# Kernel optimization log

Hardware: AMD Instinct MI355X
Metric: run time of the kernel (lower is better)

The kernel has to match this reference:

```python
import jax, jax.numpy as jnp
import numpy as np
from jax import lax

RATIO = 0.25
K = 32


def setup_inputs() -> dict:
    key = jax.random.key(0)
    ks = jax.random.split(key, 5)
    B, N, C = 16, 4096, 64
    pos = jax.random.normal(ks[0], (B, N, 3), jnp.float32)
    x = jax.random.normal(ks[1], (B, N, C), jnp.float32)

    def lin(k, fan_in, fan_out):
        return jax.random.normal(k, (fan_in, fan_out), jnp.float32) / np.sqrt(fan_in).astype(np.float32)

    W1 = lin(ks[2], C + 3, 128); b1 = jnp.zeros((128,), jnp.float32)
    W2 = lin(ks[3], 128, 128);   b2 = jnp.zeros((128,), jnp.float32)
    W3 = lin(ks[4], 128, 256);   b3 = jnp.zeros((256,), jnp.float32)
    return dict(x=x, pos=pos, W1=W1, b1=b1, W2=W2, b2=b2, W3=W3, b3=b3)


def _fps(pos, M):
    """Iterative farthest point sampling on one cloud. pos: [N,3] -> idx [M]."""
    N = pos.shape[0]

    def step(carry, _):
        dists, last = carry
        d = jnp.sum((pos - pos[last]) ** 2, axis=-1)      # [N]
        dists = jnp.minimum(dists, d)
        nxt = jnp.argmax(dists).astype(jnp.int32)
        return (dists, nxt), last

    init = (jnp.full((N,), 1e30, pos.dtype), jnp.int32(0))
    _, idx = lax.scan(step, init, None, length=M)
    return idx  # first emitted index is 0, then farthest points in order


def reference(x, pos, W1, b1, W2, b2, W3, b3):
    B, N, _ = pos.shape
    M = int(N * RATIO)

    # --- FPS sampling per cloud ---
    idx = jax.vmap(lambda p: _fps(p, M))(pos)                        # [B,M] int32
    pos_s = jnp.take_along_axis(pos, idx[..., None], axis=1)          # [B,M,3]

    # --- kNN graph: K nearest source points for each sampled centroid ---
    d2 = jnp.sum((pos_s[:, :, None, :] - pos[:, None, :, :]) ** 2, -1)  # [B,M,N]
    _, nidx = lax.top_k(-d2, K)                                       # [B,M,K]

    # --- gather neighbor features & relative positions ---
    x_j = jax.vmap(lambda xb, ib: xb[ib])(x, nidx)                    # [B,M,K,C]
    pos_j = jax.vmap(lambda pb, ib: pb[ib])(pos, nidx)                # [B,M,K,3]
    rel = pos_j - pos_s[:, :, None, :]                                # [B,M,K,3]

    # --- PointNetConv: local MLP on [x_j || rel], max aggregation ---
    msg = jnp.concatenate([x_j, rel], axis=-1)                        # [B,M,K,C+3]
    h = jax.nn.relu(msg @ W1 + b1)
    h = jax.nn.relu(h @ W2 + b2)
    h = jax.nn.relu(h @ W3 + b3)                                      # [B,M,K,256]
    out = jnp.max(h, axis=2)                                          # [B,M,256]
    return out, pos_s
```

## Files before the change

kernel.cpp:

```cpp
#include <hip/hip_runtime.h>


#define B_    16
#define N_    4096
#define M_    1024
#define AST   136
#define NWORK 240
#define NITEM (256 * 16)

typedef __bf16 bf16x8 __attribute__((ext_vector_type(8)));
typedef __bf16 bf16x4 __attribute__((ext_vector_type(4)));
typedef float  f32x4  __attribute__((ext_vector_type(4)));
typedef float  f32x2  __attribute__((ext_vector_type(2)));

__global__ __launch_bounds__(256) void prep_weights(
    const float* __restrict__ W1, const float* __restrict__ W2,
    const float* __restrict__ W3,
    __bf16* __restrict__ w1t, __bf16* __restrict__ w2t, __bf16* __restrict__ w3t) {
  const int t = blockIdx.x * 256 + threadIdx.x;
  if (t < 128 * 96) {
    const int n = t / 96, k = t % 96;
    w1t[t] = (k < 67) ? (__bf16)W1[k * 128 + n] : (__bf16)0.0f;
  }
  if (t < 128 * 128) {
    const int n = t >> 7, k = t & 127;
    w2t[t] = (__bf16)W2[k * 128 + n];
  }
  {
    const int n = t >> 7, k = t & 127;
    w3t[t] = (__bf16)W3[k * 256 + n];
  }
}

__device__ __forceinline__ f32x2 pk_sub(f32x2 a, f32x2 b) {
  f32x2 d;
  asm("v_pk_add_f32 %0, %1, %2 neg_lo:[0,1] neg_hi:[0,1]" : "=v"(d) : "v"(a), "v"(b));
  return d;
}
__device__ __forceinline__ f32x2 pk_mul(f32x2 a, f32x2 b) {
  f32x2 d;
  asm("v_pk_mul_f32 %0, %1, %2" : "=v"(d) : "v"(a), "v"(b));
  return d;
}
__device__ __forceinline__ f32x2 pk_add(f32x2 a, f32x2 b) {
  f32x2 d;
  asm("v_pk_add_f32 %0, %1, %2" : "=v"(d) : "v"(a), "v"(b));
  return d;
}

__device__ __forceinline__ double mk_key(float d, unsigned lo) {
  unsigned long long k = ((unsigned long long)__float_as_uint(d) << 32) | lo;
  return __builtin_bit_cast(double, k);
}

template <int CTRL>
__device__ __forceinline__ double dpp_max_f64(double v) {
  unsigned long long k = __builtin_bit_cast(unsigned long long, v);
  unsigned lo = (unsigned)__builtin_amdgcn_update_dpp(0, (int)(unsigned)k,         CTRL, 0xF, 0xF, true);
  unsigned hi = (unsigned)__builtin_amdgcn_update_dpp(0, (int)(unsigned)(k >> 32), CTRL, 0xF, 0xF, true);
  double p = __builtin_bit_cast(double, ((unsigned long long)hi << 32) | lo);
  return fmax(v, p);
}

union ShU {
  struct { float4 pp[N_]; unsigned long long sw[2][4]; } f;
  struct { __bf16 A[128 * AST]; __bf16 Bv[128 * AST]; } g;
};

__global__ __launch_bounds__(256) void fused_kernel(
    const float* __restrict__ pos, const float* __restrict__ x,
    const float* __restrict__ b1, const float* __restrict__ b2,
    const float* __restrict__ b3,
    const __bf16* __restrict__ w1t, const __bf16* __restrict__ w2t,
    const __bf16* __restrict__ w3t,
    int* __restrict__ ipub, int* __restrict__ ctr,
    float* __restrict__ out, float* __restrict__ pos_s) {
  __shared__ alignas(16) ShU sh;
  __shared__ int sh_item;
  const int tid = threadIdx.x;

  if (blockIdx.x < B_) {
    __builtin_amdgcn_s_setprio(3);
    const int b = blockIdx.x;
    const float* pb = pos + (size_t)b * N_ * 3;
    for (int i = tid; i < N_; i += 256)
      sh.f.pp[i] = make_float4(pb[3 * i], pb[3 * i + 1], pb[3 * i + 2], 0.0f);
    __syncthreads();

    f32x2 X2[8], Y2[8], Z2[8];
    float D[16];
    unsigned lo16[16];
    const unsigned ntid = ~(unsigned)tid;
#pragma unroll
    for (int j = 0; j < 8; j++) {
      float4 p0 = sh.f.pp[tid + ((2 * j) << 8)];
      float4 p1 = sh.f.pp[tid + ((2 * j + 1) << 8)];
      X2[j][0] = p0.x; X2[j][1] = p1.x;
      Y2[j][0] = p0.y; Y2[j][1] = p1.y;
      Z2[j][0] = p0.z; Z2[j][1] = p1.z;
      D[2 * j] = 1e30f; D[2 * j + 1] = 1e30f;
      lo16[2 * j]     = ntid - (unsigned)((2 * j) << 8);
      lo16[2 * j + 1] = ntid - (unsigned)((2 * j + 1) << 8);
    }

    float4 q = sh.f.pp[0];
    if (tid == 0) {
      __hip_atomic_store(ipub + b * M_, 1, __ATOMIC_RELAXED,
                         __HIP_MEMORY_SCOPE_AGENT);
      float* o = pos_s + (size_t)b * M_ * 3;
      o[0] = q.x; o[1] = q.y; o[2] = q.z;
    }

    for (int i = 1; i < M_; i++) {
      f32x2 qx; qx[0] = q.x; qx[1] = q.x;
      f32x2 qy; qy[0] = q.y; qy[1] = q.y;
      f32x2 qz; qz[0] = q.z; qz[1] = q.z;
      double key[16];
#pragma unroll
      for (int j = 0; j < 8; j++) {
        f32x2 dx = pk_sub(X2[j], qx);
        f32x2 dy = pk_sub(Y2[j], qy);
        f32x2 dz = pk_sub(Z2[j], qz);
        f32x2 t0 = pk_mul(dx, dx);
        f32x2 t1 = pk_mul(dy, dy);
        f32x2 s  = pk_add(t0, t1);
        f32x2 t2 = pk_mul(dz, dz);
        f32x2 d2 = pk_add(s, t2);
        D[2 * j]     = fminf(D[2 * j],     d2[0]);
        D[2 * j + 1] = fminf(D[2 * j + 1], d2[1]);
        key[2 * j]     = mk_key(D[2 * j],     lo16[2 * j]);
        key[2 * j + 1] = mk_key(D[2 * j + 1], lo16[2 * j + 1]);
      }
#pragma unroll
      for (int s = 8; s > 0; s >>= 1)
#pragma unroll
        for (int k = 0; k < s; k++)
          key[k] = fmax(key[k], key[k + s]);
      double kk = key[0];

      kk = dpp_max_f64<0xB1>(kk);
      kk = dpp_max_f64<0x4E>(kk);
      kk = dpp_max_f64<0x141>(kk);
      kk = dpp_max_f64<0x140>(kk);
      kk = dpp_max_f64<0x142>(kk);
      kk = dpp_max_f64<0x143>(kk);

      const int par = i & 1;
      if ((tid & 63) == 63)
        sh.f.sw[par][tid >> 6] = __builtin_bit_cast(unsigned long long, kk);
      asm volatile("s_waitcnt lgkmcnt(0)" ::: "memory");
      __builtin_amdgcn_s_barrier();

      const ulonglong2 v01 = *(const ulonglong2*)&sh.f.sw[par][0];
      const ulonglong2 v23 = *(const ulonglong2*)&sh.f.sw[par][2];
      const int c0 = (int)(~(unsigned)v01.x), c1 = (int)(~(unsigned)v01.y);
      const int c2 = (int)(~(unsigned)v23.x), c3 = (int)(~(unsigned)v23.y);
      float4 q0 = sh.f.pp[c0], q1 = sh.f.pp[c1], q2 = sh.f.pp[c2], q3 = sh.f.pp[c3];
      unsigned long long k01, k23; float4 q01, q23; int i01, i23;
      if (v01.y > v01.x) { k01 = v01.y; q01 = q1; i01 = c1; }
      else               { k01 = v01.x; q01 = q0; i01 = c0; }
      if (v23.y > v23.x) { k23 = v23.y; q23 = q3; i23 = c3; }
      else               { k23 = v23.x; q23 = q2; i23 = c2; }
      int cur;
      if (k23 > k01) { q = q23; cur = i23; }
      else           { q = q01; cur = i01; }

      if (tid == 0) {
        __hip_atomic_store(ipub + b * M_ + i, cur + 1, __ATOMIC_RELAXED,
                           __HIP_MEMORY_SCOPE_AGENT);
        float* o = pos_s + ((size_t)b * M_ + i) * 3;
        o[0] = q.x; o[1] = q.y; o[2] = q.z;
      }
    }
    return;
  }

  const int w    = tid >> 6;
  const int lane = tid & 63;

  for (;;) {
    if (tid == 0) sh_item = atomicAdd(ctr, 1);
    __syncthreads();
    const int it = sh_item;
    if (it >= NITEM) return;
    const int b    = it & 15;
    const int mset = it >> 4;
    const int m    = mset * 4 + w;

    __syncthreads();
    {
      const float* pb = pos + (size_t)b * N_ * 3;
      for (int i = tid; i < N_; i += 256)
        sh.f.pp[i] = make_float4(pb[3 * i], pb[3 * i + 1], pb[3 * i + 2], 0.0f);
    }
    __syncthreads();

    int ci0 = 0;
    if (lane == 0) {
      int v;
      while ((v = __hip_atomic_load(ipub + b * M_ + m, __ATOMIC_RELAXED,
                                    __HIP_MEMORY_SCOPE_AGENT)) == 0)
        __builtin_amdgcn_s_sleep(8);
      ci0 = v - 1;
    }
    const int ci = __shfl(ci0, 0);
    const float4 c = sh.f.pp[ci];

    float d2v[64];
    unsigned long long kmin = ~0ull;
#pragma unroll
    for (int t = 0; t < 64; t++) {
      const int j = t * 64 + lane;
      const float4 p = sh.f.pp[j];
      float dx = __fsub_rn(p.x, c.x);
      float dy = __fsub_rn(p.y, c.y);
      float dz = __fsub_rn(p.z, c.z);
      float d  = __fadd_rn(__fadd_rn(__fmul_rn(dx, dx), __fmul_rn(dy, dy)),
                           __fmul_rn(dz, dz));
      d2v[t] = d;
      const unsigned long long k64 =
          ((unsigned long long)__float_as_uint(d) << 32) | (unsigned int)j;
      if (k64 < kmin) kmin = k64;
    }

    unsigned long long sk = kmin;
#pragma unroll
    for (int size = 2; size <= 64; size <<= 1) {
#pragma unroll
      for (int stride = size >> 1; stride > 0; stride >>= 1) {
        const unsigned long long other = __shfl_xor(sk, stride);
        const bool up      = ((lane & size) == 0);
        const bool lowhalf = ((lane & stride) == 0);
        const bool takeMin = (up == lowhalf);
        const bool swp     = takeMin ? (other < sk) : (other > sk);
        if (swp) sk = other;
      }
    }
    const unsigned long long T0 = __shfl(sk, 31);
    const bool seeded = (kmin <= T0);

    unsigned long long rkey = (lane < 32) ? sk : ~0ull;
    unsigned long long wk   = T0;

#pragma unroll
    for (int t = 0; t < 64; t++) {
      const int j = t * 64 + lane;
      const unsigned long long k64 =
          ((unsigned long long)__float_as_uint(d2v[t]) << 32) | (unsigned int)j;
      const bool skip = seeded && (k64 == kmin);
      unsigned long long mask = __ballot((k64 < wk) && !skip);
      if (mask) {
        while (mask) {
          const int src = __ffsll((unsigned long long)mask) - 1;
          mask &= mask - 1;
          const unsigned long long cand = __shfl(k64, src);
          const int pos_i = (int)__popcll(__ballot(rkey < cand));
          const unsigned long long sh_ = __shfl_up(rkey, 1);
          if (lane < 32) {
            if (lane == pos_i)      rkey = cand;
            else if (lane > pos_i)  rkey = sh_;
          }
        }
        wk = __shfl(rkey, 31);
      }
    }
    const int njl = (int)(rkey & 0xFFFFull);
    __syncthreads();

    {
      const int rl   = lane >> 1;
      const int half = lane & 1;
      const int r    = w * 32 + rl;
      const int nj   = __shfl(njl, rl);
      const float4* xr = (const float4*)(x + ((size_t)(b * N_ + nj)) * 64 + half * 32);
      __bf16* dst = &sh.g.A[r * AST + half * 32];
#pragma unroll
      for (int t = 0; t < 8; t++) {
        float4 v = xr[t];
        bf16x4 u;
        u[0] = (__bf16)v.x; u[1] = (__bf16)v.y; u[2] = (__bf16)v.z; u[3] = (__bf16)v.w;
        *(bf16x4*)(dst + t * 4) = u;
      }
      bf16x8 z;
#pragma unroll
      for (int q2 = 0; q2 < 8; q2++) z[q2] = (__bf16)0.0f;
      if (half == 0) {
        const float* pj = pos + ((size_t)(b * N_ + nj)) * 3;
        bf16x8 u = z;
        u[0] = (__bf16)(pj[0] - c.x);
        u[1] = (__bf16)(pj[1] - c.y);
        u[2] = (__bf16)(pj[2] - c.z);
        *(bf16x8*)&sh.g.A[r * AST + 64] = u;
        *(bf16x8*)&sh.g.A[r * AST + 72] = z;
      } else {
        *(bf16x8*)&sh.g.A[r * AST + 80] = z;
        *(bf16x8*)&sh.g.A[r * AST + 88] = z;
      }
    }
    __syncthreads();

    const int lrow = lane & 15;
    const int lk8  = (lane >> 4) << 3;
    const int orow = (lane >> 4) << 2;

    {
      f32x4 acc[8][2];
#pragma unroll
      for (int n = 0; n < 2; n++) {
        const float bv = b1[(2 * w + n) * 16 + lrow];
        f32x4 a = {bv, bv, bv, bv};
#pragma unroll
        for (int rt = 0; rt < 8; rt++) acc[rt][n] = a;
      }
#pragma unroll
      for (int s = 0; s < 3; s++) {
        bf16x8 a[8];
#pragma unroll
        for (int rt = 0; rt < 8; rt++)
          a[rt] = *(const bf16x8*)&sh.g.A[(rt * 16 + lrow) * AST + s * 32 + lk8];
#pragma unroll
        for (int n = 0; n < 2; n++) {
          bf16x8 bb = *(const bf16x8*)&w1t[((2 * w + n) * 16 + lrow) * 96 + s * 32 + lk8];
#pragma unroll
          for (int rt = 0; rt < 8; rt++)
            acc[rt][n] = __builtin_amdgcn_mfma_f32_16x16x32_bf16(a[rt], bb, acc[rt][n], 0, 0, 0);
        }
      }
      __syncthreads();
#pragma unroll
      for (int n = 0; n < 2; n++)
#pragma unroll
        for (int rt = 0; rt < 8; rt++)
#pragma unroll
          for (int j = 0; j < 4; j++)
            sh.g.Bv[(rt * 16 + orow + j) * AST + (2 * w + n) * 16 + lrow] =
                (__bf16)fmaxf(acc[rt][n][j], 0.0f);
    }
    __syncthreads();

    {
      f32x4 acc[8][2];
#pragma unroll
      for (int n = 0; n < 2; n++) {
        const float bv = b2[(2 * w + n) * 16 + lrow];
        f32x4 a = {bv, bv, bv, bv};
#pragma unroll
        for (int rt = 0; rt < 8; rt++) acc[rt][n] = a;
      }
#pragma unroll
      for (int s = 0; s < 4; s++) {
        bf16x8 a[8];
#pragma unroll
        for (int rt = 0; rt < 8; rt++)
          a[rt] = *(const bf16x8*)&sh.g.Bv[(rt * 16 + lrow) * AST + s * 32 + lk8];
#pragma unroll
        for (int n = 0; n < 2; n++) {
          bf16x8 bb = *(const bf16x8*)&w2t[((2 * w + n) * 16 + lrow) * 128 + s * 32 + lk8];
#pragma unroll
          for (int rt = 0; rt < 8; rt++)
            acc[rt][n] = __builtin_amdgcn_mfma_f32_16x16x32_bf16(a[rt], bb, acc[rt][n], 0, 0, 0);
        }
      }
      __syncthreads();
#pragma unroll
      for (int n = 0; n < 2; n++)
#pragma unroll
        for (int rt = 0; rt < 8; rt++)
#pragma unroll
          for (int j = 0; j < 4; j++)
            sh.g.A[(rt * 16 + orow + j) * AST + (2 * w + n) * 16 + lrow] =
                (__bf16)fmaxf(acc[rt][n][j], 0.0f);
    }
    __syncthreads();

#pragma unroll
    for (int np = 0; np < 2; np++) {
      f32x4 acc[8][2];
#pragma unroll
      for (int n = 0; n < 2; n++) {
        const float bv = b3[(4 * w + 2 * np + n) * 16 + lrow];
        f32x4 a = {bv, bv, bv, bv};
#pragma unroll
        for (int rt = 0; rt < 8; rt++) acc[rt][n] = a;
      }
#pragma unroll
      for (int s = 0; s < 4; s++) {
        bf16x8 a[8];
#pragma unroll
        for (int rt = 0; rt < 8; rt++)
          a[rt] = *(const bf16x8*)&sh.g.A[(rt * 16 + lrow) * AST + s * 32 + lk8];
#pragma unroll
        for (int n = 0; n < 2; n++) {
          bf16x8 bb = *(const bf16x8*)&w3t[((4 * w + 2 * np + n) * 16 + lrow) * 128 + s * 32 + lk8];
#pragma unroll
          for (int rt = 0; rt < 8; rt++)
            acc[rt][n] = __builtin_amdgcn_mfma_f32_16x16x32_bf16(a[rt], bb, acc[rt][n], 0, 0, 0);
        }
      }
#pragma unroll
      for (int ccc = 0; ccc < 4; ccc++) {
#pragma unroll
        for (int n = 0; n < 2; n++) {
          f32x4 a0 = acc[2 * ccc][n], a1 = acc[2 * ccc + 1][n];
          float v = fmaxf(fmaxf(fmaxf(a0[0], a0[1]), fmaxf(a0[2], a0[3])),
                          fmaxf(fmaxf(a1[0], a1[1]), fmaxf(a1[2], a1[3])));
          v = fmaxf(v, __shfl_xor(v, 16));
          v = fmaxf(v, __shfl_xor(v, 32));
          v = fmaxf(v, 0.0f);
          if (lane < 16)
            out[((size_t)(b * M_ + mset * 4 + ccc)) * 256 + (4 * w + 2 * np + n) * 16 + lane] = v;
        }
      }
    }
  }
}

extern "C" void kernel_launch(void* const* d_in, const int* in_sizes, int n_in,
                              void* d_out, int out_size, void* d_ws, size_t ws_size,
                              hipStream_t stream) {
  const float* x   = (const float*)d_in[0];
  const float* pos = (const float*)d_in[1];
  const float* W1  = (const float*)d_in[2];
  const float* b1  = (const float*)d_in[3];
  const float* W2  = (const float*)d_in[4];
  const float* b2  = (const float*)d_in[5];
  const float* W3  = (const float*)d_in[6];
  const float* b3  = (const float*)d_in[7];

  float* out   = (float*)d_out;
  float* pos_s = out + (size_t)B_ * M_ * 256;

  char* ws = (char*)d_ws;
  int*    ipub = (int*)ws;
  int*    ctr  = (int*)(ws + 65536);
  __bf16* w1t  = (__bf16*)(ws + 65792);
  __bf16* w2t  = (__bf16*)(ws + 90368);
  __bf16* w3t  = (__bf16*)(ws + 123136);

  hipMemsetAsync(ws, 0, 65540, stream);
  prep_weights<<<dim3(128), dim3(256), 0, stream>>>(W1, W2, W3, w1t, w2t, w3t);
  fused_kernel<<<dim3(B_ + NWORK), dim3(256), 0, stream>>>(
      pos, x, b1, b2, b3, w1t, w2t, w3t, ipub, ctr, out, pos_s);
}
```

Baseline: 597.8 us.

## Process final centroid group in FPS block and simplify winner selection

Measured after the change: 594.2 us. About the same (-0.6%).

```diff
diff --git a/kernel.cpp b/kernel.cpp
--- a/kernel.cpp
+++ b/kernel.cpp
@@ -6,7 +6,7 @@
 #define M_    1024
 #define AST   136
 #define NWORK 240
-#define NITEM (256 * 16)
+#define NITEM (255 * 16)
 
 typedef __bf16 bf16x8 __attribute__((ext_vector_type(8)));
 typedef __bf16 bf16x4 __attribute__((ext_vector_type(4)));
@@ -66,6 +66,225 @@
   struct { float4 pp[N_]; unsigned long long sw[2][4]; } f;
   struct { __bf16 A[128 * AST]; __bf16 Bv[128 * AST]; } g;
 };
+
+__device__ __forceinline__ void process_item(
+    ShU& sh, int tid, int b, int mset, int ci,
+    const float* __restrict__ x, const float* __restrict__ pos,
+    const float* __restrict__ b1, const float* __restrict__ b2,
+    const float* __restrict__ b3,
+    const __bf16* __restrict__ w1t, const __bf16* __restrict__ w2t,
+    const __bf16* __restrict__ w3t, float* __restrict__ out) {
+  const int w    = tid >> 6;
+  const int lane = tid & 63;
+  const float4 c = sh.f.pp[ci];
+
+  float d2v[64];
+  unsigned long long kmin = ~0ull;
+#pragma unroll
+  for (int t = 0; t < 64; t++) {
+    const int j = t * 64 + lane;
+    const float4 p = sh.f.pp[j];
+    float dx = __fsub_rn(p.x, c.x);
+    float dy = __fsub_rn(p.y, c.y);
+    float dz = __fsub_rn(p.z, c.z);
+    float d  = __fadd_rn(__fadd_rn(__fmul_rn(dx, dx), __fmul_rn(dy, dy)),
+                         __fmul_rn(dz, dz));
+    d2v[t] = d;
+    const unsigned long long k64 =
+        ((unsigned long long)__float_as_uint(d) << 32) | (unsigned int)j;
+    if (k64 < kmin) kmin = k64;
+  }
+
+  unsigned long long sk = kmin;
+#pragma unroll
+  for (int size = 2; size <= 64; size <<= 1) {
+#pragma unroll
+    for (int stride = size >> 1; stride > 0; stride >>= 1) {
+      const unsigned long long other = __shfl_xor(sk, stride);
+      const bool up      = ((lane & size) == 0);
+      const bool lowhalf = ((lane & stride) == 0);
+      const bool takeMin = (up == lowhalf);
+      const bool swp     = takeMin ? (other < sk) : (other > sk);
+      if (swp) sk = other;
+    }
+  }
+  const unsigned long long T0 = __shfl(sk, 31);
+  const bool seeded = (kmin <= T0);
+
+  unsigned long long rkey = (lane < 32) ? sk : ~0ull;
+  unsigned long long wk   = T0;
+
+#pragma unroll
+  for (int t = 0; t < 64; t++) {
+    const int j = t * 64 + lane;
+    const unsigned long long k64 =
+        ((unsigned long long)__float_as_uint(d2v[t]) << 32) | (unsigned int)j;
+    const bool skip = seeded && (k64 == kmin);
+    unsigned long long mask = __ballot((k64 < wk) && !skip);
+    if (mask) {
+      while (mask) {
+        const int src = __ffsll((unsigned long long)mask) - 1;
+        mask &= mask - 1;
+        const unsigned long long cand = __shfl(k64, src);
+        const int pos_i = (int)__popcll(__ballot(rkey < cand));
+        const unsigned long long sh_ = __shfl_up(rkey, 1);
+        if (lane < 32) {
+          if (lane == pos_i)      rkey = cand;
+          else if (lane > pos_i)  rkey = sh_;
+        }
+      }
+      wk = __shfl(rkey, 31);
+    }
+  }
+  const int njl = (int)(rkey & 0xFFFFull);
+  __syncthreads();
+
+  {
+    const int rl   = lane >> 1;
+    const int half = lane & 1;
+    const int r    = w * 32 + rl;
+    const int nj   = __shfl(njl, rl);
+    const float4* xr = (const float4*)(x + ((size_t)(b * N_ + nj)) * 64 + half * 32);
+    __bf16* dst = &sh.g.A[r * AST + half * 32];
+#pragma unroll
+    for (int t = 0; t < 8; t++) {
+      float4 v = xr[t];
+      bf16x4 u;
+      u[0] = (__bf16)v.x; u[1] = (__bf16)v.y; u[2] = (__bf16)v.z; u[3] = (__bf16)v.w;
+      *(bf16x4*)(dst + t * 4) = u;
+    }
+    bf16x8 z;
+#pragma unroll
+    for (int q2 = 0; q2 < 8; q2++) z[q2] = (__bf16)0.0f;
+    if (half == 0) {
+      const float* pj = pos + ((size_t)(b * N_ + nj)) * 3;
+      bf16x8 u = z;
+      u[0] = (__bf16)(pj[0] - c.x);
+      u[1] = (__bf16)(pj[1] - c.y);
+      u[2] = (__bf16)(pj[2] - c.z);
+      *(bf16x8*)&sh.g.A[r * AST + 64] = u;
+      *(bf16x8*)&sh.g.A[r * AST + 72] = z;
+    } else {
+      *(bf16x8*)&sh.g.A[r * AST + 80] = z;
+      *(bf16x8*)&sh.g.A[r * AST + 88] = z;
+    }
+  }
+  __syncthreads();
+
+  const int lrow = lane & 15;
+  const int lk8  = (lane >> 4) << 3;
+  const int orow = (lane >> 4) << 2;
+
+  {
+    f32x4 acc[8][2];
+#pragma unroll
+    for (int n = 0; n < 2; n++) {
+      const float bv = b1[(2 * w + n) * 16 + lrow];
+      f32x4 a = {bv, bv, bv, bv};
+#pragma unroll
+      for (int rt = 0; rt < 8; rt++) acc[rt][n] = a;
+    }
+#pragma unroll
+    for (int s = 0; s < 3; s++) {
+      bf16x8 a[8];
+#pragma unroll
+      for (int rt = 0; rt < 8; rt++)
+        a[rt] = *(const bf16x8*)&sh.g.A[(rt * 16 + lrow) * AST + s * 32 + lk8];
+#pragma unroll
+      for (int n = 0; n < 2; n++) {
+        bf16x8 bb = *(const bf16x8*)&w1t[((2 * w + n) * 16 + lrow) * 96 + s * 32 + lk8];
+#pragma unroll
+        for (int rt = 0; rt < 8; rt++)
+          acc[rt][n] = __builtin_amdgcn_mfma_f32_16x16x32_bf16(a[rt], bb, acc[rt][n], 0, 0, 0);
+      }
+    }
+    __syncthreads();
+#pragma unroll
+    for (int n = 0; n < 2; n++)
+#pragma unroll
+      for (int rt = 0; rt < 8; rt++)
+#pragma unroll
+        for (int j = 0; j < 4; j++)
+          sh.g.Bv[(rt * 16 + orow + j) * AST + (2 * w + n) * 16 + lrow] =
+              (__bf16)fmaxf(acc[rt][n][j], 0.0f);
+  }
+  __syncthreads();
+
+  {
+    f32x4 acc[8][2];
+#pragma unroll
+    for (int n = 0; n < 2; n++) {
+      const float bv = b2[(2 * w + n) * 16 + lrow];
+      f32x4 a = {bv, bv, bv, bv};
+#pragma unroll
+      for (int rt = 0; rt < 8; rt++) acc[rt][n] = a;
+    }
+#pragma unroll
+    for (int s = 0; s < 4; s++) {
+      bf16x8 a[8];
+#pragma unroll
+      for (int rt = 0; rt < 8; rt++)
+        a[rt] = *(const bf16x8*)&sh.g.Bv[(rt * 16 + lrow) * AST + s * 32 + lk8];
+#pragma unroll
+      for (int n = 0; n < 2; n++) {
+        bf16x8 bb = *(const bf16x8*)&w2t[((2 * w + n) * 16 + lrow) * 128 + s * 32 + lk8];
+#pragma unroll
+        for (int rt = 0; rt < 8; rt++)
+          acc[rt][n] = __builtin_amdgcn_mfma_f32_16x16x32_bf16(a[rt], bb, acc[rt][n], 0, 0, 0);
+      }
+    }
+    __syncthreads();
+#pragma unroll
+    for (int n = 0; n < 2; n++)
+#pragma unroll
+      for (int rt = 0; rt < 8; rt++)
+#pragma unroll
+        for (int j = 0; j < 4; j++)
+          sh.g.A[(rt * 16 + orow + j) * AST + (2 * w + n) * 16 + lrow] =
+              (__bf16)fmaxf(acc[rt][n][j], 0.0f);
+  }
+  __syncthreads();
+
+#pragma unroll
+  for (int np = 0; np < 2; np++) {
+    f32x4 acc[8][2];
+#pragma unroll
+    for (int n = 0; n < 2; n++) {
+      const float bv = b3[(4 * w + 2 * np + n) * 16 + lrow];
+      f32x4 a = {bv, bv, bv, bv};
+#pragma unroll
+      for (int rt = 0; rt < 8; rt++) acc[rt][n] = a;
+    }
+#pragma unroll
+    for (int s = 0; s < 4; s++) {
+      bf16x8 a[8];
+#pragma unroll
+      for (int rt = 0; rt < 8; rt++)
+        a[rt] = *(const bf16x8*)&sh.g.A[(rt * 16 + lrow) * AST + s * 32 + lk8];
+#pragma unroll
+      for (int n = 0; n < 2; n++) {
+        bf16x8 bb = *(const bf16x8*)&w3t[((4 * w + 2 * np + n) * 16 + lrow) * 128 + s * 32 + lk8];
+#pragma unroll
+        for (int rt = 0; rt < 8; rt++)
+          acc[rt][n] = __builtin_amdgcn_mfma_f32_16x16x32_bf16(a[rt], bb, acc[rt][n], 0, 0, 0);
+      }
+    }
+#pragma unroll
+    for (int ccc = 0; ccc < 4; ccc++) {
+#pragma unroll
+      for (int n = 0; n < 2; n++) {
+        f32x4 a0 = acc[2 * ccc][n], a1 = acc[2 * ccc + 1][n];
+        float v = fmaxf(fmaxf(fmaxf(a0[0], a0[1]), fmaxf(a0[2], a0[3])),
+                        fmaxf(fmaxf(a1[0], a1[1]), fmaxf(a1[2], a1[3])));
+        v = fmaxf(v, __shfl_xor(v, 16));
+        v = fmaxf(v, __shfl_xor(v, 32));
+        v = fmaxf(v, 0.0f);
+        if (lane < 16)
+          out[((size_t)(b * M_ + mset * 4 + ccc)) * 256 + (4 * w + 2 * np + n) * 16 + lane] = v;
+      }
+    }
+  }
+}
 
 __global__ __launch_bounds__(256) void fused_kernel(
     const float* __restrict__ pos, const float* __restrict__ x,
@@ -111,6 +330,7 @@
       o[0] = q.x; o[1] = q.y; o[2] = q.z;
     }
 
+    int l0 = 0, l1 = 0, l2 = 0, l3 = 0;
     for (int i = 1; i < M_; i++) {
       f32x2 qx; qx[0] = q.x; qx[1] = q.x;
       f32x2 qy; qy[0] = q.y; qy[1] = q.y;
@@ -151,20 +371,19 @@
       asm volatile("s_waitcnt lgkmcnt(0)" ::: "memory");
       __builtin_amdgcn_s_barrier();
 
-      const ulonglong2 v01 = *(const ulonglong2*)&sh.f.sw[par][0];
-      const ulonglong2 v23 = *(const ulonglong2*)&sh.f.sw[par][2];
-      const int c0 = (int)(~(unsigned)v01.x), c1 = (int)(~(unsigned)v01.y);
-      const int c2 = (int)(~(unsigned)v23.x), c3 = (int)(~(unsigned)v23.y);
-      float4 q0 = sh.f.pp[c0], q1 = sh.f.pp[c1], q2 = sh.f.pp[c2], q3 = sh.f.pp[c3];
-      unsigned long long k01, k23; float4 q01, q23; int i01, i23;
-      if (v01.y > v01.x) { k01 = v01.y; q01 = q1; i01 = c1; }
-      else               { k01 = v01.x; q01 = q0; i01 = c0; }
-      if (v23.y > v23.x) { k23 = v23.y; q23 = q3; i23 = c3; }
-      else               { k23 = v23.x; q23 = q2; i23 = c2; }
-      int cur;
-      if (k23 > k01) { q = q23; cur = i23; }
-      else           { q = q01; cur = i01; }
-
+      const double2 w01 = *(const double2*)&sh.f.sw[par][0];
+      const double2 w23 = *(const double2*)&sh.f.sw[par][2];
+      const double kwin = fmax(fmax(w01.x, w01.y), fmax(w23.x, w23.y));
+      const unsigned long long kwb = __builtin_bit_cast(unsigned long long, kwin);
+      const int cur = (int)(~(unsigned)kwb);
+      q = sh.f.pp[cur];
+
+      if (i >= M_ - 4) {
+        if      (i == M_ - 4) l0 = cur;
+        else if (i == M_ - 3) l1 = cur;
+        else if (i == M_ - 2) l2 = cur;
+        else                  l3 = cur;
+      }
       if (tid == 0) {
         __hip_atomic_store(ipub + b * M_ + i, cur + 1, __ATOMIC_RELAXED,
                            __HIP_MEMORY_SCOPE_AGENT);
@@ -172,11 +391,19 @@
         o[0] = q.x; o[1] = q.y; o[2] = q.z;
       }
     }
+
+    const int w = tid >> 6;
+    int ci;
+    if      (w == 0) ci = l0;
+    else if (w == 1) ci = l1;
+    else if (w == 2) ci = l2;
+    else             ci = l3;
+    process_item(sh, tid, b, 255, ci, x, pos, b1, b2, b3, w1t, w2t, w3t, out);
     return;
   }
 
+  const int lane = tid & 63;
   const int w    = tid >> 6;
-  const int lane = tid & 63;
 
   for (;;) {
     if (tid == 0) sh_item = atomicAdd(ctr, 1);
@@ -204,214 +431,8 @@
       ci0 = v - 1;
     }
     const int ci = __shfl(ci0, 0);
-    const float4 c = sh.f.pp[ci];
-
-    float d2v[64];
-    unsigned long long kmin = ~0ull;
-#pragma unroll
-    for (int t = 0; t < 64; t++) {
-      const int j = t * 64 + lane;
-      const float4 p = sh.f.pp[j];
-      float dx = __fsub_rn(p.x, c.x);
-      float dy = __fsub_rn(p.y, c.y);
-      float dz = __fsub_rn(p.z, c.z);
-      float d  = __fadd_rn(__fadd_rn(__fmul_rn(dx, dx), __fmul_rn(dy, dy)),
-                           __fmul_rn(dz, dz));
-      d2v[t] = d;
-      const unsigned long long k64 =
-          ((unsigned long long)__float_as_uint(d) << 32) | (unsigned int)j;
-      if (k64 < kmin) kmin = k64;
-    }
-
-    unsigned long long sk = kmin;
-#pragma unroll
-    for (int size = 2; size <= 64; size <<= 1) {
-#pragma unroll
-      for (int stride = size >> 1; stride > 0; stride >>= 1) {
-        const unsigned long long other = __shfl_xor(sk, stride);
-        const bool up      = ((lane & size) == 0);
-        const bool lowhalf = ((lane & stride) == 0);
-        const bool takeMin = (up == lowhalf);
-        const bool swp     = takeMin ? (other < sk) : (other > sk);
-        if (swp) sk = other;
-      }
-    }
-    const unsigned long long T0 = __shfl(sk, 31);
-    const bool seeded = (kmin <= T0);
-
-    unsigned long long rkey = (lane < 32) ? sk : ~0ull;
-    unsigned long long wk   = T0;
-
-#pragma unroll
-    for (int t = 0; t < 64; t++) {
-      const int j = t * 64 + lane;
-      const unsigned long long k64 =
-          ((unsigned long long)__float_as_uint(d2v[t]) << 32) | (unsigned int)j;
-      const bool skip = seeded && (k64 == kmin);
-      unsigned long long mask = __ballot((k64 < wk) && !skip);
-      if (mask) {
-        while (mask) {
-          const int src = __ffsll((unsigned long long)mask) - 1;
-          mask &= mask - 1;
-          const unsigned long long cand = __shfl(k64, src);
-          const int pos_i = (int)__popcll(__ballot(rkey < cand));
-          const unsigned long long sh_ = __shfl_up(rkey, 1);
-          if (lane < 32) {
-            if (lane == pos_i)      rkey = cand;
-            else if (lane > pos_i)  rkey = sh_;
-          }
-        }
-        wk = __shfl(rkey, 31);
-      }
-    }
-    const int njl = (int)(rkey & 0xFFFFull);
-    __syncthreads();
-
-    {
-      const int rl   = lane >> 1;
-      const int half = lane & 1;
-      const int r    = w * 32 + rl;
-      const int nj   = __shfl(njl, rl);
-      const float4* xr = (const float4*)(x + ((size_t)(b * N_ + nj)) * 64 + half * 32);
-      __bf16* dst = &sh.g.A[r * AST + half * 32];
-#pragma unroll
-      for (int t = 0; t < 8; t++) {
-        float4 v = xr[t];
-        bf16x4 u;
-        u[0] = (__bf16)v.x; u[1] = (__bf16)v.y; u[2] = (__bf16)v.z; u[3] = (__bf16)v.w;
-        *(bf16x4*)(dst + t * 4) = u;
-      }
-      bf16x8 z;
-#pragma unroll
-      for (int q2 = 0; q2 < 8; q2++) z[q2] = (__bf16)0.0f;
-      if (half == 0) {
-        const float* pj = pos + ((size_t)(b * N_ + nj)) * 3;
-        bf16x8 u = z;
-        u[0] = (__bf16)(pj[0] - c.x);
-        u[1] = (__bf16)(pj[1] - c.y);
-        u[2] = (__bf16)(pj[2] - c.z);
-        *(bf16x8*)&sh.g.A[r * AST + 64] = u;
-        *(bf16x8*)&sh.g.A[r * AST + 72] = z;
-      } else {
-        *(bf16x8*)&sh.g.A[r * AST + 80] = z;
-        *(bf16x8*)&sh.g.A[r * AST + 88] = z;
-      }
-    }
-    __syncthreads();
-
-    const int lrow = lane & 15;
-    const int lk8  = (lane >> 4) << 3;
-    const int orow = (lane >> 4) << 2;
-
-    {
-      f32x4 acc[8][2];
-#pragma unroll
-      for (int n = 0; n < 2; n++) {
-        const float bv = b1[(2 * w + n) * 16 + lrow];
-        f32x4 a = {bv, bv, bv, bv};
-#pragma unroll
-        for (int rt = 0; rt < 8; rt++) acc[rt][n] = a;
-      }
-#pragma unroll
-      for (int s = 0; s < 3; s++) {
-        bf16x8 a[8];
-#pragma unroll
-        for (int rt = 0; rt < 8; rt++)
-          a[rt] = *(const bf16x8*)&sh.g.A[(rt * 16 + lrow) * AST + s * 32 + lk8];
-#pragma unroll
-        for (int n = 0; n < 2; n++) {
-          bf16x8 bb = *(const bf16x8*)&w1t[((2 * w + n) * 16 + lrow) * 96 + s * 32 + lk8];
-#pragma unroll
-          for (int rt = 0; rt < 8; rt++)
-            acc[rt][n] = __builtin_amdgcn_mfma_f32_16x16x32_bf16(a[rt], bb, acc[rt][n], 0, 0, 0);
-        }
-      }
-      __syncthreads();
-#pragma unroll
-      for (int n = 0; n < 2; n++)
-#pragma unroll
-        for (int rt = 0; rt < 8; rt++)
-#pragma unroll
-          for (int j = 0; j < 4; j++)
-            sh.g.Bv[(rt * 16 + orow + j) * AST + (2 * w + n) * 16 + lrow] =
-                (__bf16)fmaxf(acc[rt][n][j], 0.0f);
-    }
-    __syncthreads();
-
-    {
-      f32x4 acc[8][2];
-#pragma unroll
-      for (int n = 0; n < 2; n++) {
-        const float bv = b2[(2 * w + n) * 16 + lrow];
-        f32x4 a = {bv, bv, bv, bv};
-#pragma unroll
-        for (int rt = 0; rt < 8; rt++) acc[rt][n] = a;
-      }
-#pragma unroll
-      for (int s = 0; s < 4; s++) {
-        bf16x8 a[8];
-#pragma unroll
-        for (int rt = 0; rt < 8; rt++)
-          a[rt] = *(const bf16x8*)&sh.g.Bv[(rt * 16 + lrow) * AST + s * 32 + lk8];
-#pragma unroll
-        for (int n = 0; n < 2; n++) {
-          bf16x8 bb = *(const bf16x8*)&w2t[((2 * w + n) * 16 + lrow) * 128 + s * 32 + lk8];
-#pragma unroll
-          for (int rt = 0; rt < 8; rt++)
-            acc[rt][n] = __builtin_amdgcn_mfma_f32_16x16x32_bf16(a[rt], bb, acc[rt][n], 0, 0, 0);
-        }
-      }
-      __syncthreads();
-#pragma unroll
-      for (int n = 0; n < 2; n++)
-#pragma unroll
-        for (int rt = 0; rt < 8; rt++)
-#pragma unroll
-          for (int j = 0; j < 4; j++)
-            sh.g.A[(rt * 16 + orow + j) * AST + (2 * w + n) * 16 + lrow] =
-                (__bf16)fmaxf(acc[rt][n][j], 0.0f);
-    }
-    __syncthreads();
-
-#pragma unroll
-    for (int np = 0; np < 2; np++) {
-      f32x4 acc[8][2];
-#pragma unroll
-      for (int n = 0; n < 2; n++) {
-        const float bv = b3[(4 * w + 2 * np + n) * 16 + lrow];
-        f32x4 a = {bv, bv, bv, bv};
-#pragma unroll
-        for (int rt = 0; rt < 8; rt++) acc[rt][n] = a;
-      }
-#pragma unroll
-      for (int s = 0; s < 4; s++) {
-        bf16x8 a[8];
-#pragma unroll
-        for (int rt = 0; rt < 8; rt++)
-          a[rt] = *(const bf16x8*)&sh.g.A[(rt * 16 + lrow) * AST + s * 32 + lk8];
-#pragma unroll
-        for (int n = 0; n < 2; n++) {
-          bf16x8 bb = *(const bf16x8*)&w3t[((4 * w + 2 * np + n) * 16 + lrow) * 128 + s * 32 + lk8];
-#pragma unroll
-          for (int rt = 0; rt < 8; rt++)
-            acc[rt][n] = __builtin_amdgcn_mfma_f32_16x16x32_bf16(a[rt], bb, acc[rt][n], 0, 0, 0);
-        }
-      }
-#pragma unroll
-      for (int ccc = 0; ccc < 4; ccc++) {
-#pragma unroll
-        for (int n = 0; n < 2; n++) {
-          f32x4 a0 = acc[2 * ccc][n], a1 = acc[2 * ccc + 1][n];
-          float v = fmaxf(fmaxf(fmaxf(a0[0], a0[1]), fmaxf(a0[2], a0[3])),
-                          fmaxf(fmaxf(a1[0], a1[1]), fmaxf(a1[2], a1[3])));
-          v = fmaxf(v, __shfl_xor(v, 16));
-          v = fmaxf(v, __shfl_xor(v, 32));
-          v = fmaxf(v, 0.0f);
-          if (lane < 16)
-            out[((size_t)(b * M_ + mset * 4 + ccc)) * 256 + (4 * w + 2 * np + n) * 16 + lane] = v;
-        }
-      }
-    }
+
+    process_item(sh, tid, b, mset, ci, x, pos, b1, b2, b3, w1t, w2t, w3t, out);
   }
 }
 
```
